# Kernel optimization log

Measured on AMD Instinct MI355X. Metric: run time of the kernel, lower is better.

## Reference

```python
import jax, jax.numpy as jnp
import numpy as np

B, H0, W0, DIM, HEADS, WS, SHIFT = 32, 56, 56, 384, 12, 7, 3
MLP_HID = DIM * 4
N = WS * WS  # tokens per window

def _rel_pos_index(ws):
    coords = np.stack(np.meshgrid(np.arange(ws), np.arange(ws), indexing='ij')).reshape(2, -1)
    rel = (coords[:, :, None] - coords[:, None, :]).transpose(1, 2, 0)
    rel[:, :, 0] += ws - 1
    rel[:, :, 1] += ws - 1
    rel[:, :, 0] *= 2 * ws - 1
    return rel.sum(-1)  # (N, N) int

REL_IDX = _rel_pos_index(WS)

def _shift_mask(H, W, ws, shift):
    # standard Swin SW-MSA mask: 0 within same region, -100 across regions
    img = np.zeros((H, W), dtype=np.int32)
    cnt = 0
    for hs in (slice(0, -ws), slice(-ws, -shift), slice(-shift, None)):
        for wsl in (slice(0, -ws), slice(-ws, -shift), slice(-shift, None)):
            img[hs, wsl] = cnt
            cnt += 1
    mw = img.reshape(H // ws, ws, W // ws, ws).transpose(0, 2, 1, 3).reshape(-1, ws * ws)
    return np.where(mw[:, None, :] != mw[:, :, None], -100.0, 0.0).astype(np.float32)  # (nW, N, N)

MASK = _shift_mask(H0, W0, WS, SHIFT)

def _ln(x, g, b, eps=1e-5):
    m = x.mean(-1, keepdims=True)
    v = ((x - m) ** 2).mean(-1, keepdims=True)
    return (x - m) / jnp.sqrt(v + eps) * g + b

def setup_inputs():
    key = jax.random.key(0)
    ks = jax.random.split(key, 8)
    d = {}
    d['x'] = jax.random.normal(ks[0], (B, H0 * W0, DIM), jnp.float32)
    d['H'], d['W'] = H0, W0
    d['norm1_g'] = jnp.ones((DIM,), jnp.float32)
    d['norm1_b'] = jnp.zeros((DIM,), jnp.float32)
    d['qkv_w'] = jax.random.normal(ks[1], (3 * DIM, DIM), jnp.float32) * 0.02
    d['qkv_b'] = jnp.zeros((3 * DIM,), jnp.float32)
    d['rpb_table'] = jax.random.normal(ks[2], ((2 * WS - 1) ** 2, HEADS), jnp.float32) * 0.02
    d['proj_w'] = jax.random.normal(ks[3], (DIM, DIM), jnp.float32) * 0.02
    d['proj_b'] = jnp.zeros((DIM,), jnp.float32)
    d['norm2_g'] = jnp.ones((DIM,), jnp.float32)
    d['norm2_b'] = jnp.zeros((DIM,), jnp.float32)
    d['fc1_w'] = jax.random.normal(ks[4], (MLP_HID, DIM), jnp.float32) * 0.02
    d['fc1_b'] = jnp.zeros((MLP_HID,), jnp.float32)
    d['fc2_w'] = jax.random.normal(ks[5], (DIM, MLP_HID), jnp.float32) * 0.02
    d['fc2_b'] = jnp.zeros((DIM,), jnp.float32)
    return d

def reference(x, H, W, norm1_g, norm1_b, qkv_w, qkv_b, rpb_table, proj_w, proj_b, norm2_g, norm2_b, fc1_w, fc1_b, fc2_w, fc2_b):
    Bx, L, C = x.shape
    hd = C // HEADS
    scale = hd ** -0.5
    shortcut = x
    xn = _ln(x, norm1_g, norm1_b).reshape(Bx, H, W, C)
    if SHIFT > 0:
        xn = jnp.roll(xn, (-SHIFT, -SHIFT), axis=(1, 2))
    nWh, nWw = H // WS, W // WS
    nW = nWh * nWw
    # window partition: (B, H, W, C) -> (B*nW, N, C)
    xw = xn.reshape(Bx, nWh, WS, nWw, WS, C).transpose(0, 1, 3, 2, 4, 5).reshape(-1, N, C)
    qkv = (xw @ qkv_w.T + qkv_b).reshape(-1, N, 3, HEADS, hd).transpose(2, 0, 3, 1, 4)
    q, k, v = qkv[0] * scale, qkv[1], qkv[2]  # (B*nW, HEADS, N, hd)
    attn = jnp.einsum('bhnd,bhmd->bhnm', q, k)
    bias = rpb_table[jnp.asarray(REL_IDX.reshape(-1))].reshape(N, N, HEADS).transpose(2, 0, 1)
    attn = attn + bias[None]
    if SHIFT > 0:
        attn = attn.reshape(Bx, nW, HEADS, N, N) + jnp.asarray(MASK)[None, :, None]
        attn = attn.reshape(-1, HEADS, N, N)
    attn = jax.nn.softmax(attn, axis=-1)
    out = jnp.einsum('bhnm,bhmd->bhnd', attn, v).transpose(0, 2, 1, 3).reshape(-1, N, C)
    out = out @ proj_w.T + proj_b
    # window reverse: (B*nW, N, C) -> (B, H, W, C)
    xr = out.reshape(Bx, nWh, nWw, WS, WS, C).transpose(0, 1, 3, 2, 4, 5).reshape(Bx, H, W, C)
    if SHIFT > 0:
        xr = jnp.roll(xr, (SHIFT, SHIFT), axis=(1, 2))
    x = shortcut + xr.reshape(Bx, L, C)
    h = _ln(x, norm2_g, norm2_b)
    h = jax.nn.gelu(h @ fc1_w.T + fc1_b, approximate=False)  # nn.GELU default = exact erf
    h = h @ fc2_w.T + fc2_b
    return x + h
```

## Files before the change

### kernel.cpp

```cpp
#include <hip/hip_runtime.h>
#include <hip/hip_bf16.h>

#define C_DIM   384
#define HEADS   12
#define HDIM    32
#define NTOK    49
#define TOT_WIN 2048
#define M_TOK   100352
#define QKV_N   1152
#define MLP_N   1536
#define SHIFT_V 3

typedef __bf16 bf16x8_t __attribute__((ext_vector_type(8)));
typedef float  f32x4_t  __attribute__((ext_vector_type(4)));

__device__ inline float b2f(ushort u) {
    union { unsigned u; float f; } p; p.u = ((unsigned)u) << 16; return p.f;
}
__device__ inline ushort f2b(float f) {
    union { float f; unsigned u; } p; p.f = f;
    unsigned r = p.u + 0x7FFF + ((p.u >> 16) & 1);
    return (ushort)(r >> 16);
}
__device__ inline float ldin(const void* p, size_t i, int dt) {
    return dt ? b2f(((const ushort*)p)[i]) : ((const float*)p)[i];
}

__device__ inline void gload_lds16(const ushort* g, ushort* l) {
    __builtin_amdgcn_global_load_lds(
        (__attribute__((address_space(1))) void*)const_cast<ushort*>(g),
        (__attribute__((address_space(3))) void*)l, 16, 0, 0);
}

__device__ inline int win2tok(int grow) {
    int widx = grow / 49, tok = grow - widx * 49;
    int b = widx >> 6, w_ = widx & 63;
    int wh = w_ >> 3, ww = w_ & 7;
    int r = tok / 7, c = tok - r * 7;
    int h = wh * 7 + r + SHIFT_V; if (h >= 56) h -= 56;
    int wc = ww * 7 + c + SHIFT_V; if (wc >= 56) wc -= 56;
    return b * 3136 + h * 56 + wc;
}

__global__ void sniff_kernel(const ushort* x16, int* flag) {
    const int tid = threadIdx.x;
    int cnt = 0;
    for (int i = tid; i < 4096; i += 256) {
        ushort u = x16[2 * i];
        int e = (u >> 7) & 0xFF;
        if ((u & 0x7FFF) == 0 || (e >= 107 && e <= 147)) cnt++;
    }
    __shared__ int ss[256];
    ss[tid] = cnt; __syncthreads();
    for (int s = 128; s; s >>= 1) { if (tid < s) ss[tid] += ss[tid + s]; __syncthreads(); }
    if (tid == 0) *flag = (ss[0] >= 2048) ? 1 : 0;
}

__global__ void cvt_w_kernel(const void* src, ushort* dst, int n, const int* flagp) {
    const int dt = *flagp;
    for (int i = blockIdx.x * blockDim.x + threadIdx.x; i < n; i += gridDim.x * blockDim.x)
        dst[i] = dt ? ((const ushort*)src)[i] : f2b(((const float*)src)[i]);
}

__global__ void cvt_p_kernel(const void* n1g, const void* n1b, const void* qkvb,
                             const void* projb, const void* n2g, const void* n2b,
                             const void* fc1b, const void* fc2b, const void* rpb,
                             float* prm, const int* flagp) {
    const int dt = *flagp;
    for (int i = threadIdx.x; i < 7020; i += 256) {
        float v;
        if      (i < 384)  v = ldin(n1g,  i,        dt);
        else if (i < 768)  v = ldin(n1b,  i - 384,  dt);
        else if (i < 1920) v = ldin(qkvb, i - 768,  dt);
        else if (i < 2304) v = ldin(projb,i - 1920, dt);
        else if (i < 2688) v = ldin(n2g,  i - 2304, dt);
        else if (i < 3072) v = ldin(n2b,  i - 2688, dt);
        else if (i < 4608) v = ldin(fc1b, i - 3072, dt);
        else if (i < 4992) v = ldin(fc2b, i - 4608, dt);
        else               v = ldin(rpb,  i - 4992, dt);
        prm[i] = v;
    }
}

template<int MODE>
__global__ __launch_bounds__(256) void ln_kernel(
    const void* __restrict__ x, const float* __restrict__ g,
    const float* __restrict__ b, ushort* __restrict__ out,
    const int* flagp, int moff)
{
    const int dt = *flagp;
    const int wid = threadIdx.x >> 6, lane = threadIdx.x & 63;
    const int m = blockIdx.x * 4 + wid;
    const int src = (MODE == 0) ? win2tok(moff + m) : (moff + m);

    float v[6]; float s = 0.f, sq = 0.f;
    #pragma unroll
    for (int k = 0; k < 6; ++k) {
        v[k] = ldin(x, (size_t)src * C_DIM + lane + 64 * k, dt);
        s += v[k]; sq += v[k] * v[k];
    }
    #pragma unroll
    for (int off = 32; off; off >>= 1) {
        s  += __shfl_xor(s,  off, 64);
        sq += __shfl_xor(sq, off, 64);
    }
    float mean = s * (1.f / 384.f);
    float var  = sq * (1.f / 384.f) - mean * mean;
    float rstd = rsqrtf(var + 1e-5f);
    #pragma unroll
    for (int k = 0; k < 6; ++k) {
        int col = lane + 64 * k;
        out[(size_t)m * C_DIM + col] =
            f2b((v[k] - mean) * rstd * g[col] + b[col]);
    }
}

template<int MODE>
__global__ __launch_bounds__(256, 2) void gemm_bt(
    const ushort* __restrict__ A, const ushort* __restrict__ W,
    const float* __restrict__ bias, ushort* outb, void* outv,
    const void* resid, const int* flagp, int N, int K, int Mrows, int moff)
{
    __shared__ __align__(16) ushort As[2][128 * 32];
    __shared__ __align__(16) ushort Bs[2][128 * 32];

    const int dt   = *flagp;
    const int tid  = threadIdx.x;
    const int wid  = tid >> 6;
    const int lane = tid & 63;
    const int bm = blockIdx.y * 128;
    const int bn = blockIdx.x * 128;
    const int wm = (wid >> 1) * 64;
    const int wn = (wid & 1) * 64;
    const int lrow = lane & 15;
    const int lk   = (lane >> 4) << 3;

    const int c0    = wid * 2;
    const int srow0 = c0 * 16 + (lane >> 2);
    const int srow1 = srow0 + 16;
    const int skoff = (lane & 3) << 3;

    const int ar0 = (bm + srow0 < Mrows) ? (bm + srow0) : (Mrows - 1);
    const int ar1 = (bm + srow1 < Mrows) ? (bm + srow1) : (Mrows - 1);

    const ushort* pa0 = A + (size_t)ar0 * K + skoff;
    const ushort* pa1 = A + (size_t)ar1 * K + skoff;
    const ushort* pb0 = W + (size_t)(bn + srow0) * K + skoff;
    const ushort* pb1 = W + (size_t)(bn + srow1) * K + skoff;

    float biasf[4]; int coln[4];
    #pragma unroll
    for (int n = 0; n < 4; ++n) {
        coln[n] = bn + wn + n * 16 + lrow;
        biasf[n] = bias[coln[n]];
    }

    f32x4_t acc[4][4];
    #pragma unroll
    for (int m = 0; m < 4; ++m)
        #pragma unroll
        for (int n = 0; n < 4; ++n) acc[m][n] = (f32x4_t){0.f, 0.f, 0.f, 0.f};

    const int nk = K >> 5;
    gload_lds16(pa0, As[0] + (c0)     * 512);
    gload_lds16(pa1, As[0] + (c0 + 1) * 512);
    gload_lds16(pb0, Bs[0] + (c0)     * 512);
    gload_lds16(pb1, Bs[0] + (c0 + 1) * 512);

    int cur = 0;
    for (int kt = 0; kt < nk; ++kt) {
        if (kt + 1 < nk) {
            const int nxt = cur ^ 1;
            const int k1 = (kt + 1) << 5;
            gload_lds16(pa0 + k1, As[nxt] + (c0)     * 512);
            gload_lds16(pa1 + k1, As[nxt] + (c0 + 1) * 512);
            gload_lds16(pb0 + k1, Bs[nxt] + (c0)     * 512);
            gload_lds16(pb1 + k1, Bs[nxt] + (c0 + 1) * 512);
            __builtin_amdgcn_sched_barrier(0);
            asm volatile("s_waitcnt vmcnt(4)" ::: "memory");
        } else {
            asm volatile("s_waitcnt vmcnt(0)" ::: "memory");
        }
        __builtin_amdgcn_s_barrier();
        __builtin_amdgcn_sched_barrier(0);

        bf16x8_t af[4], bfr[4];
        #pragma unroll
        for (int m = 0; m < 4; ++m)
            af[m] = *(const bf16x8_t*)&As[cur][(wm + m * 16 + lrow) * 32 + lk];
        #pragma unroll
        for (int n = 0; n < 4; ++n)
            bfr[n] = *(const bf16x8_t*)&Bs[cur][(wn + n * 16 + lrow) * 32 + lk];
        #pragma unroll
        for (int m = 0; m < 4; ++m)
            #pragma unroll
            for (int n = 0; n < 4; ++n)
                acc[m][n] = __builtin_amdgcn_mfma_f32_16x16x32_bf16(
                    af[m], bfr[n], acc[m][n], 0, 0, 0);

        __builtin_amdgcn_sched_barrier(0);
        __builtin_amdgcn_s_barrier();
        cur ^= 1;
    }

    const int rbase = bm + wm + ((lane >> 4) << 2);
    #pragma unroll
    for (int m = 0; m < 4; ++m) {
        #pragma unroll
        for (int j = 0; j < 4; ++j) {
            int grow = rbase + m * 16 + j;
            if (grow >= Mrows) continue;
            #pragma unroll
            for (int n = 0; n < 4; ++n) {
                float v = acc[m][n][j] + biasf[n];
                if (MODE == 0) {
                    outb[(size_t)grow * N + coln[n]] = f2b(v);
                } else if (MODE == 2) {
                    v = 0.5f * v * (1.0f + erff(v * 0.70710678118654752f));
                    outb[(size_t)grow * N + coln[n]] = f2b(v);
                } else {
                    size_t orow = (MODE == 1) ? (size_t)win2tok(moff + grow)
                                              : (size_t)(moff + grow);
                    size_t oidx = orow * (size_t)N + coln[n];
                    float r = v + ldin(resid, oidx, dt);
                    if (dt) ((ushort*)outv)[oidx] = f2b(r);
                    else    ((float*) outv)[oidx] = r;
                }
            }
        }
    }
}

__global__ __launch_bounds__(256) void attn_kernel(
    const ushort* __restrict__ qkv, const float* __restrict__ rpb,
    ushort* __restrict__ out, int win_off)
{
    __shared__ __align__(16) ushort Pl[4][64 * 64];
    __shared__ __align__(16) ushort Vtl[4][32 * 64];

    const int tid = threadIdx.x, wid = tid >> 6, lane = tid & 63;
    const int lo = lane & 15, hi = lane >> 4;
    const int widx = blockIdx.x;
    const int w_ = (win_off + widx) & 63;
    const int wh = w_ >> 3, ww = w_ & 7;
    const bool edge = (wh == 7) || (ww == 7);

    char* P  = (char*)Pl[wid];
    char* Vw = (char*)Vtl[wid];

    int qr[4], qc[4], rq[4];
    #pragma unroll
    for (int n = 0; n < 4; ++n) {
        int q = n * 16 + lo; if (q > 48) q = 48;
        qr[n] = q / 7; qc[n] = q - qr[n] * 7;
        int gh = wh * 7 + qr[n], gw = ww * 7 + qc[n];
        rq[n] = (gh < 49 ? 0 : (gh < 53 ? 1 : 2)) * 3 + (gw < 49 ? 0 : (gw < 53 ? 1 : 2));
    }

    for (int h = wid; h < HEADS; h += 4) {
        const size_t hb = (size_t)widx * 49 * QKV_N + h * HDIM;

        bf16x8_t kf[4], qf[4];
        #pragma unroll
        for (int t = 0; t < 4; ++t) {
            int r = t * 16 + lo;
            bf16x8_t z = {};
            kf[t] = z; qf[t] = z;
            if (r < 49) {
                kf[t] = *(const bf16x8_t*)(qkv + hb + (size_t)r * QKV_N + 384 + hi * 8);
                qf[t] = *(const bf16x8_t*)(qkv + hb + (size_t)r * QKV_N + hi * 8);
            }
        }

        {
            const int kk = lane;
            union { bf16x8_t v; ushort u[8]; } vv[4];
            #pragma unroll
            for (int c = 0; c < 4; ++c) {
                bf16x8_t z = {};
                vv[c].v = (kk < 49) ? *(const bf16x8_t*)(qkv + hb + (size_t)kk * QKV_N + 768 + c * 8)
                                    : z;
            }
            #pragma unroll
            for (int d = 0; d < 32; ++d) {
                int byo = (d * 128 + kk * 2) ^ ((d & 7) << 4);
                *(ushort*)(Vw + byo) = vv[d >> 3].u[d & 7];
            }
        }

        f32x4_t St[4][4];
        #pragma unroll
        for (int m = 0; m < 4; ++m)
            #pragma unroll
            for (int n = 0; n < 4; ++n) St[m][n] = (f32x4_t){0.f, 0.f, 0.f, 0.f};
        #pragma unroll
        for (int m = 0; m < 4; ++m)
            #pragma unroll
            for (int n = 0; n < 4; ++n)
                St[m][n] = __builtin_amdgcn_mfma_f32_16x16x32_bf16(kf[m], qf[n], St[m][n], 0, 0, 0);

        #pragma unroll
        for (int m = 0; m < 4; ++m) {
            #pragma unroll
            for (int j = 0; j < 4; ++j) {
                const int kk = m * 16 + hi * 4 + j;
                const int kcl = (kk > 48) ? 48 : kk;
                const int kr = kcl / 7, kc = kcl - kr * 7;
                int rk = 0;
                if (edge) {
                    int gh = wh * 7 + kr, gw = ww * 7 + kc;
                    rk = (gh < 49 ? 0 : (gh < 53 ? 1 : 2)) * 3 + (gw < 49 ? 0 : (gw < 53 ? 1 : 2));
                }
                #pragma unroll
                for (int n = 0; n < 4; ++n) {
                    int idx = (qr[n] - kr + 6) * 13 + (qc[n] - kc + 6);
                    float v = St[m][n][j] * 0.17677669529663687f + rpb[idx * 12 + h];
                    if (edge && (rq[n] != rk)) v -= 100.f;
                    if (kk > 48) v = -1e30f;
                    St[m][n][j] = v;
                }
            }
        }

        float sm[4];
        #pragma unroll
        for (int n = 0; n < 4; ++n) {
            float mv = St[0][n][0];
            #pragma unroll
            for (int m = 0; m < 4; ++m)
                #pragma unroll
                for (int j = 0; j < 4; ++j) mv = fmaxf(mv, St[m][n][j]);
            mv = fmaxf(mv, __shfl_xor(mv, 16, 64));
            mv = fmaxf(mv, __shfl_xor(mv, 32, 64));
            float sv = 0.f;
            #pragma unroll
            for (int m = 0; m < 4; ++m)
                #pragma unroll
                for (int j = 0; j < 4; ++j) {
                    float e = __expf(St[m][n][j] - mv);
                    St[m][n][j] = e; sv += e;
                }
            sv += __shfl_xor(sv, 16, 64);
            sv += __shfl_xor(sv, 32, 64);
            sm[n] = 1.f / sv;
        }

        #pragma unroll
        for (int m = 0; m < 4; ++m) {
            #pragma unroll
            for (int n = 0; n < 4; ++n) {
                union { ushort4 u4; __bf16 b[4]; } pk;
                #pragma unroll
                for (int j = 0; j < 4; ++j) pk.b[j] = (__bf16)(St[m][n][j] * sm[n]);
                int byo = ((n * 16 + lo) * 128 + (m * 16 + hi * 4) * 2) ^ ((lo & 7) << 4);
                *(ushort4*)(P + byo) = pk.u4;
            }
        }

        f32x4_t Oa[4][2];
        #pragma unroll
        for (int mt = 0; mt < 4; ++mt)
            #pragma unroll
            for (int nt = 0; nt < 2; ++nt) Oa[mt][nt] = (f32x4_t){0.f, 0.f, 0.f, 0.f};
        #pragma unroll
        for (int s = 0; s < 2; ++s) {
            bf16x8_t vf[2];
            #pragma unroll
            for (int nt = 0; nt < 2; ++nt) {
                int byo = ((nt * 16 + lo) * 128 + s * 64 + hi * 16) ^ ((lo & 7) << 4);
                vf[nt] = *(const bf16x8_t*)(Vw + byo);
            }
            #pragma unroll
            for (int mt = 0; mt < 4; ++mt) {
                int byo = ((mt * 16 + lo) * 128 + s * 64 + hi * 16) ^ ((lo & 7) << 4);
                bf16x8_t pf = *(const bf16x8_t*)(P + byo);
                #pragma unroll
                for (int nt = 0; nt < 2; ++nt)
                    Oa[mt][nt] = __builtin_amdgcn_mfma_f32_16x16x32_bf16(pf, vf[nt], Oa[mt][nt], 0, 0, 0);
            }
        }

        #pragma unroll
        for (int mt = 0; mt < 4; ++mt) {
            #pragma unroll
            for (int j = 0; j < 4; ++j) {
                int q = mt * 16 + hi * 4 + j;
                if (q < 49) {
                    size_t ro = ((size_t)(widx * 49 + q)) * C_DIM + h * HDIM;
                    #pragma unroll
                    for (int nt = 0; nt < 2; ++nt)
                        out[ro + nt * 16 + lo] = f2b(Oa[mt][nt][j]);
                }
            }
        }
    }
}

extern "C" void kernel_launch(void* const* d_in, const int* in_sizes, int n_in,
                              void* d_out, int out_size, void* d_ws, size_t ws_size,
                              hipStream_t stream)
{
    const void* x      = d_in[0];
    const void* n1g    = d_in[3];
    const void* n1b    = d_in[4];
    const void* qkv_w  = d_in[5];
    const void* qkv_b  = d_in[6];
    const void* rpb    = d_in[7];
    const void* proj_w = d_in[8];
    const void* proj_b = d_in[9];
    const void* n2g    = d_in[10];
    const void* n2b    = d_in[11];
    const void* fc1_w  = d_in[12];
    const void* fc1_b  = d_in[13];
    const void* fc2_w  = d_in[14];
    const void* fc2_b  = d_in[15];

    int*    flagp = (int*)d_ws;
    float*  prm   = (float*)((char*)d_ws + 256);
    ushort* wq    = (ushort*)((char*)d_ws + 28416);
    ushort* wp    = wq + 442368;
    ushort* w1m   = wp + 147456;
    ushort* w2m   = w1m + 589824;
    const size_t WSTATIC = 3567360;

    int nc = 64;
    const int opts[7] = {1, 2, 4, 8, 16, 32, 64};
    for (int i = 0; i < 7; ++i) {
        size_t need = WSTATIC + ((size_t)M_TOK / opts[i]) * 3840ull;
        if (need <= ws_size) { nc = opts[i]; break; }
    }
    const int wins_pc = TOT_WIN / nc;
    const int rows_pc = wins_pc * NTOK;
    const int gx      = (rows_pc + 127) / 128;

    ushort* ws0 = (ushort*)((char*)d_ws + WSTATIC);
    ushort* ws1 = ws0 + (size_t)rows_pc * C_DIM;

    sniff_kernel<<<1, 256, 0, stream>>>((const ushort*)x, flagp);
    cvt_p_kernel<<<1, 256, 0, stream>>>(n1g, n1b, qkv_b, proj_b, n2g, n2b,
                                        fc1_b, fc2_b, rpb, prm, flagp);
    cvt_w_kernel<<<432, 256, 0, stream>>>(qkv_w,  wq,  442368, flagp);
    cvt_w_kernel<<<144, 256, 0, stream>>>(proj_w, wp,  147456, flagp);
    cvt_w_kernel<<<576, 256, 0, stream>>>(fc1_w,  w1m, 589824, flagp);
    cvt_w_kernel<<<576, 256, 0, stream>>>(fc2_w,  w2m, 589824, flagp);

    const float* b_qkv = prm + 768;
    const float* b_prj = prm + 1920;
    const float* b_fc1 = prm + 3072;
    const float* b_fc2 = prm + 4608;
    const float* rpb_c = prm + 4992;

    for (int c = 0; c < nc; ++c) {
        const int moff = c * rows_pc;
        ln_kernel<0><<<rows_pc / 4, 256, 0, stream>>>(x, prm + 0, prm + 384, ws0, flagp, moff);
        gemm_bt<0><<<dim3(9, gx), 256, 0, stream>>>(
            ws0, wq, b_qkv, ws1, nullptr, nullptr, flagp, QKV_N, C_DIM, rows_pc, 0);
        attn_kernel<<<wins_pc, 256, 0, stream>>>(ws1, rpb_c, ws0, c * wins_pc);
        gemm_bt<1><<<dim3(3, gx), 256, 0, stream>>>(
            ws0, wp, b_prj, nullptr, d_out, x, flagp, C_DIM, C_DIM, rows_pc, moff);
    }

    for (int c = 0; c < nc; ++c) {
        const int moff = c * rows_pc;
        ln_kernel<1><<<rows_pc / 4, 256, 0, stream>>>(d_out, prm + 2304, prm + 2688, ws0, flagp, moff);
        gemm_bt<2><<<dim3(12, gx), 256, 0, stream>>>(
            ws0, w1m, b_fc1, ws1, nullptr, nullptr, flagp, MLP_N, C_DIM, rows_pc, 0);
        gemm_bt<3><<<dim3(3, gx), 256, 0, stream>>>(
            ws1, w2m, b_fc2, nullptr, d_out, d_out, flagp, C_DIM, MLP_N, rows_pc, moff);
    }
}
```

Measured before the change: 1.151 ms.

## Triple-buffer GEMM LDS pipeline and keep intermediate residual in bf16 scratch

The GEMM main loop moves from double to triple buffering, prefetching two K-tiles ahead so global loads overlap more MFMA work. The attention-output residual is now written as bf16 into a dedicated workspace buffer instead of d_out. LN2 and the fc2 residual read that buffer, which halves the bytes moved when the output is fp32. The cost is extra LDS per block, which may lower occupancy, an extra bf16 rounding of the intermediate residual, and a larger workspace requirement that can force more chunks.

```diff
diff --git a/kernel.cpp b/kernel.cpp
--- a/kernel.cpp
+++ b/kernel.cpp
@@ -96,7 +96,8 @@
     float v[6]; float s = 0.f, sq = 0.f;
     #pragma unroll
     for (int k = 0; k < 6; ++k) {
-        v[k] = ldin(x, (size_t)src * C_DIM + lane + 64 * k, dt);
+        size_t idx = (size_t)src * C_DIM + lane + 64 * k;
+        v[k] = (MODE == 2) ? b2f(((const ushort*)x)[idx]) : ldin(x, idx, dt);
         s += v[k]; sq += v[k] * v[k];
     }
     #pragma unroll
@@ -121,8 +122,8 @@
     const float* __restrict__ bias, ushort* outb, void* outv,
     const void* resid, const int* flagp, int N, int K, int Mrows, int moff)
 {
-    __shared__ __align__(16) ushort As[2][128 * 32];
-    __shared__ __align__(16) ushort Bs[2][128 * 32];
+    __shared__ __align__(16) ushort As[3][128 * 32];
+    __shared__ __align__(16) ushort Bs[3][128 * 32];
 
     const int dt   = *flagp;
     const int tid  = threadIdx.x;
@@ -162,20 +163,26 @@
         for (int n = 0; n < 4; ++n) acc[m][n] = (f32x4_t){0.f, 0.f, 0.f, 0.f};
 
     const int nk = K >> 5;
-    gload_lds16(pa0, As[0] + (c0)     * 512);
-    gload_lds16(pa1, As[0] + (c0 + 1) * 512);
-    gload_lds16(pb0, Bs[0] + (c0)     * 512);
-    gload_lds16(pb1, Bs[0] + (c0 + 1) * 512);
-
-    int cur = 0;
+    gload_lds16(pa0,      As[0] + (c0)     * 512);
+    gload_lds16(pa1,      As[0] + (c0 + 1) * 512);
+    gload_lds16(pb0,      Bs[0] + (c0)     * 512);
+    gload_lds16(pb1,      Bs[0] + (c0 + 1) * 512);
+    gload_lds16(pa0 + 32, As[1] + (c0)     * 512);
+    gload_lds16(pa1 + 32, As[1] + (c0 + 1) * 512);
+    gload_lds16(pb0 + 32, Bs[1] + (c0)     * 512);
+    gload_lds16(pb1 + 32, Bs[1] + (c0 + 1) * 512);
+
+    int cur = 0, stg = 2;
     for (int kt = 0; kt < nk; ++kt) {
-        if (kt + 1 < nk) {
-            const int nxt = cur ^ 1;
-            const int k1 = (kt + 1) << 5;
-            gload_lds16(pa0 + k1, As[nxt] + (c0)     * 512);
-            gload_lds16(pa1 + k1, As[nxt] + (c0 + 1) * 512);
-            gload_lds16(pb0 + k1, Bs[nxt] + (c0)     * 512);
-            gload_lds16(pb1 + k1, Bs[nxt] + (c0 + 1) * 512);
+        if (kt + 2 < nk) {
+            const int k2 = (kt + 2) << 5;
+            gload_lds16(pa0 + k2, As[stg] + (c0)     * 512);
+            gload_lds16(pa1 + k2, As[stg] + (c0 + 1) * 512);
+            gload_lds16(pb0 + k2, Bs[stg] + (c0)     * 512);
+            gload_lds16(pb1 + k2, Bs[stg] + (c0 + 1) * 512);
+            __builtin_amdgcn_sched_barrier(0);
+            asm volatile("s_waitcnt vmcnt(8)" ::: "memory");
+        } else if (kt + 1 < nk) {
             __builtin_amdgcn_sched_barrier(0);
             asm volatile("s_waitcnt vmcnt(4)" ::: "memory");
         } else {
@@ -200,7 +207,8 @@
 
         __builtin_amdgcn_sched_barrier(0);
         __builtin_amdgcn_s_barrier();
-        cur ^= 1;
+        cur = (cur == 2) ? 0 : cur + 1;
+        stg = (stg == 2) ? 0 : stg + 1;
     }
 
     const int rbase = bm + wm + ((lane >> 4) << 2);
@@ -218,11 +226,12 @@
                 } else if (MODE == 2) {
                     v = 0.5f * v * (1.0f + erff(v * 0.70710678118654752f));
                     outb[(size_t)grow * N + coln[n]] = f2b(v);
+                } else if (MODE == 1) {
+                    size_t oidx = (size_t)win2tok(moff + grow) * (size_t)N + coln[n];
+                    outb[oidx] = f2b(v + ldin(resid, oidx, dt));
                 } else {
-                    size_t orow = (MODE == 1) ? (size_t)win2tok(moff + grow)
-                                              : (size_t)(moff + grow);
-                    size_t oidx = orow * (size_t)N + coln[n];
-                    float r = v + ldin(resid, oidx, dt);
+                    size_t oidx = (size_t)(moff + grow) * (size_t)N + coln[n];
+                    float r = v + b2f(((const ushort*)resid)[oidx]);
                     if (dt) ((ushort*)outv)[oidx] = f2b(r);
                     else    ((float*) outv)[oidx] = r;
                 }
@@ -422,18 +431,20 @@
     ushort* w1m   = wp + 147456;
     ushort* w2m   = w1m + 589824;
     const size_t WSTATIC = 3567360;
+    const size_t X2B_B   = 77070336ull;
 
     int nc = 64;
     const int opts[7] = {1, 2, 4, 8, 16, 32, 64};
     for (int i = 0; i < 7; ++i) {
-        size_t need = WSTATIC + ((size_t)M_TOK / opts[i]) * 3840ull;
+        size_t need = WSTATIC + X2B_B + ((size_t)M_TOK / opts[i]) * 3840ull;
         if (need <= ws_size) { nc = opts[i]; break; }
     }
     const int wins_pc = TOT_WIN / nc;
     const int rows_pc = wins_pc * NTOK;
     const int gx      = (rows_pc + 127) / 128;
 
-    ushort* ws0 = (ushort*)((char*)d_ws + WSTATIC);
+    ushort* x2b = (ushort*)((char*)d_ws + WSTATIC);
+    ushort* ws0 = x2b + (size_t)M_TOK * C_DIM;
     ushort* ws1 = ws0 + (size_t)rows_pc * C_DIM;
 
     sniff_kernel<<<1, 256, 0, stream>>>((const ushort*)x, flagp);
@@ -457,15 +468,15 @@
             ws0, wq, b_qkv, ws1, nullptr, nullptr, flagp, QKV_N, C_DIM, rows_pc, 0);
         attn_kernel<<<wins_pc, 256, 0, stream>>>(ws1, rpb_c, ws0, c * wins_pc);
         gemm_bt<1><<<dim3(3, gx), 256, 0, stream>>>(
-            ws0, wp, b_prj, nullptr, d_out, x, flagp, C_DIM, C_DIM, rows_pc, moff);
+            ws0, wp, b_prj, x2b, nullptr, x, flagp, C_DIM, C_DIM, rows_pc, moff);
     }
 
     for (int c = 0; c < nc; ++c) {
         const int moff = c * rows_pc;
-        ln_kernel<1><<<rows_pc / 4, 256, 0, stream>>>(d_out, prm + 2304, prm + 2688, ws0, flagp, moff);
+        ln_kernel<2><<<rows_pc / 4, 256, 0, stream>>>(x2b, prm + 2304, prm + 2688, ws0, flagp, moff);
         gemm_bt<2><<<dim3(12, gx), 256, 0, stream>>>(
             ws0, w1m, b_fc1, ws1, nullptr, nullptr, flagp, MLP_N, C_DIM, rows_pc, 0);
         gemm_bt<3><<<dim3(3, gx), 256, 0, stream>>>(
-            ws1, w2m, b_fc2, nullptr, d_out, d_out, flagp, C_DIM, MLP_N, rows_pc, moff);
-    }
-}
+            ws1, w2m, b_fc2, nullptr, d_out, x2b, flagp, C_DIM, MLP_N, rows_pc, moff);
+    }
+}
```

Result: no change. 1.156 ms (+0.4%).
